# Performance work log

Measured on AMD Instinct MI355X. Metric: run time of the kernel, lower is better.

Reference implementation:

```python
import jax, jax.numpy as jnp
import numpy as np

B, C_IN, IMG, P = 64, 3, 224, 16
GRID = IMG // P              # 14
N_PATCH = GRID * GRID        # 196
S = N_PATCH + 1              # 197 tokens incl CLS
D, H, HD = 768, 12, 64
DFF = 3072
L, PRUNE_AFTER = 12, 4
RATIO, EPS = 0.5, 1e-6
NEG = -1e30                  # additive mask value (softmax weight -> exactly 0 in fp32)
N_CLASSES = 1000
N_KEEP = max(1, int(S * (1.0 - RATIO)))  # 98, matches torch topk count


def _ln(x, g, b):
    m = x.mean(-1, keepdims=True)
    v = ((x - m) ** 2).mean(-1, keepdims=True)
    return (x - m) * jax.lax.rsqrt(v + EPS) * g + b


def _attn(x, qkv_w, qkv_b, proj_w, proj_b, amask):
    Bx, N, C = x.shape
    qkv = (x @ qkv_w.T + qkv_b).reshape(Bx, N, 3, H, HD).transpose(2, 0, 3, 1, 4)
    q, k, v = qkv[0], qkv[1], qkv[2]            # [B,H,N,HD]
    s = jnp.einsum('bhqd,bhkd->bhqk', q, k) * (HD ** -0.5)
    if amask is not None:
        s = s + amask                            # [B,1,1,N] broadcast
    a = jax.nn.softmax(s, axis=-1)
    o = jnp.einsum('bhqk,bhkd->bhqd', a, v).transpose(0, 2, 1, 3).reshape(Bx, N, C)
    return o @ proj_w.T + proj_b


def _block(x, i, p, amask=None):
    h = _ln(x, p['ln1_g'][i], p['ln1_b'][i])
    x = x + _attn(h, p['qkv_w'][i], p['qkv_b'][i], p['proj_w'][i], p['proj_b'][i], amask)
    h = _ln(x, p['ln2_g'][i], p['ln2_b'][i])
    h = jax.nn.gelu(h @ p['fc1_w'][i].T + p['fc1_b'][i], approximate=False)
    x = x + (h @ p['fc2_w'][i].T + p['fc2_b'][i])
    return x


def _forward(images, patch_w, patch_b, cls_token, pos_embed,
             ln1_g, ln1_b, qkv_w, qkv_b, proj_w, proj_b,
             ln2_g, ln2_b, fc1_w, fc1_b, fc2_w, fc2_b,
             norm_g, norm_b, head_w, head_b):
    p = dict(ln1_g=ln1_g, ln1_b=ln1_b, qkv_w=qkv_w, qkv_b=qkv_b,
             proj_w=proj_w, proj_b=proj_b, ln2_g=ln2_g, ln2_b=ln2_b,
             fc1_w=fc1_w, fc1_b=fc1_b, fc2_w=fc2_w, fc2_b=fc2_b)
    Bx = images.shape[0]
    # patch embed: non-overlapping 16x16 conv == patch extract + matmul
    patches = images.reshape(Bx, C_IN, GRID, P, GRID, P).transpose(0, 2, 4, 1, 3, 5)
    patches = patches.reshape(Bx, N_PATCH, C_IN * P * P)
    x = patches @ patch_w.reshape(D, -1).T + patch_b          # [B,196,768]
    x = jnp.concatenate([jnp.broadcast_to(cls_token, (Bx, 1, D)), x], axis=1)
    x = x + pos_embed                                          # [B,197,768]
    # early dense blocks
    for i in range(PRUNE_AFTER):
        x = _block(x, i, p)
    # _threshold_prune: topk on token norms, CLS always kept
    scores = jnp.linalg.norm(x, axis=-1)                       # [B,S]
    _, idx = jax.lax.top_k(scores, N_KEEP)                     # [B,98]
    mask = jnp.zeros((Bx, S), bool).at[jnp.arange(Bx)[:, None], idx].set(True)
    mask = mask.at[:, 0].set(True)
    # _gather_pad: kept tokens compacted to front (original order), zeros after
    order = jnp.argsort(~mask, axis=1, stable=True)            # True positions first
    x_pad = jnp.take_along_axis(x, order[:, :, None], axis=1)
    attn_m = jnp.take_along_axis(mask, order, axis=1)          # [B,S] True-prefix
    x_pad = x_pad * attn_m[:, :, None]
    amask = jnp.where(attn_m, 0.0, NEG).astype(x.dtype)[:, None, None, :]  # [B,1,1,S]
    # late masked blocks
    for i in range(PRUNE_AFTER, L):
        x_pad = _block(x_pad, i, p, amask)
    cls = _ln(x_pad[:, 0], norm_g, norm_b)
    return cls @ head_w.T + head_b                             # [B,1000]


def setup_inputs():
    key = jax.random.key(0)
    ks = iter(jax.random.split(key, 32))
    r = lambda shape: jax.random.normal(next(ks), shape, jnp.float32) * 0.02
    return {
        'images': jax.random.normal(next(ks), (B, C_IN, IMG, IMG), jnp.float32),
        'patch_w': r((D, C_IN, P, P)),
        'patch_b': r((D,)),
        'cls_token': r((1, 1, D)),
        'pos_embed': r((1, S, D)),
        'ln1_g': jnp.ones((L, D), jnp.float32),
        'ln1_b': jnp.zeros((L, D), jnp.float32),
        'qkv_w': r((L, 3 * D, D)),
        'qkv_b': r((L, 3 * D)),
        'proj_w': r((L, D, D)),
        'proj_b': r((L, D)),
        'ln2_g': jnp.ones((L, D), jnp.float32),
        'ln2_b': jnp.zeros((L, D), jnp.float32),
        'fc1_w': r((L, DFF, D)),
        'fc1_b': r((L, DFF)),
        'fc2_w': r((L, D, DFF)),
        'fc2_b': r((L, D)),
        'norm_g': jnp.ones((D,), jnp.float32),
        'norm_b': jnp.zeros((D,), jnp.float32),
        'head_w': r((N_CLASSES, D)),
        'head_b': r((N_CLASSES,)),
    }


def reference(images, patch_w, patch_b, cls_token, pos_embed,
              ln1_g, ln1_b, qkv_w, qkv_b, proj_w, proj_b,
              ln2_g, ln2_b, fc1_w, fc1_b, fc2_w, fc2_b,
              norm_g, norm_b, head_w, head_b):
    return _forward(images, patch_w, patch_b, cls_token, pos_embed,
                    ln1_g, ln1_b, qkv_w, qkv_b, proj_w, proj_b,
                    ln2_g, ln2_b, fc1_w, fc1_b, fc2_w, fc2_b,
                    norm_g, norm_b, head_w, head_b)
```

## Files before the change

### kernel.cpp

```cpp
#include <hip/hip_runtime.h>
#include <cstdint>
#include <cstddef>


#define NTOK 197
#define NB 64
#define NHEAD 12
#define SL 99

typedef __attribute__((ext_vector_type(8))) _Float16 half8;
typedef __attribute__((ext_vector_type(4))) float f32x4;
typedef __attribute__((ext_vector_type(4))) unsigned short us4;

#define DEV static __device__ __forceinline__

DEV unsigned short f2h(float f) {
    union { _Float16 h; unsigned short u; } v;
    v.h = (_Float16)f;
    return v.u;
}
DEV float h2f(unsigned short u) {
    union { _Float16 h; unsigned short u; } v;
    v.u = u;
    return (float)v.h;
}

DEV void gload16(const void* g, void* l) {
    __builtin_amdgcn_global_load_lds((const __attribute__((address_space(1))) unsigned int*)g,
                                     (__attribute__((address_space(3))) unsigned int*)l, 16, 0, 0);
}

__global__ __launch_bounds__(256) void cvt_layer_k(const float* __restrict__ qw,
                                                   const float* __restrict__ pw,
                                                   const float* __restrict__ f1,
                                                   const float* __restrict__ f2,
                                                   unsigned short* __restrict__ dh)
{
    size_t t = (size_t)blockIdx.x * 256 + threadIdx.x;
    size_t e = t * 4;
    const float* src; size_t loc;
    if (e < 1769472)      { src = qw; loc = e; }
    else if (e < 2359296) { src = pw; loc = e - 1769472; }
    else if (e < 4718592) { src = f1; loc = e - 2359296; }
    else                  { src = f2; loc = e - 4718592; }
    float4 v = *(const float4*)(src + loc);
    us4 hi; hi.x = f2h(v.x); hi.y = f2h(v.y); hi.z = f2h(v.z); hi.w = f2h(v.w);
    *(us4*)(dh + e) = hi;
}

__global__ __launch_bounds__(256) void cvt_simple_k(const float* __restrict__ src,
                                                    unsigned short* __restrict__ dh, int n4)
{
    int t = blockIdx.x * 256 + threadIdx.x;
    if (t >= n4) return;
    size_t e = (size_t)t * 4;
    float4 v = *(const float4*)(src + e);
    us4 hi; hi.x = f2h(v.x); hi.y = f2h(v.y); hi.z = f2h(v.z); hi.w = f2h(v.w);
    *(us4*)(dh + e) = hi;
}

__global__ __launch_bounds__(256) void patch_extract2_k(const float* __restrict__ img,
                                                        unsigned short* __restrict__ ph)
{
    int pi = blockIdx.x, b = blockIdx.y;
    int gy = pi / 14, gx = pi % 14;
    size_t obase = ((size_t)b * 196 + pi) * 768;
    for (int f = threadIdx.x; f < 768; f += 256) {
        int c = f >> 8, py = (f >> 4) & 15, px = f & 15;
        float v = img[(((size_t)b * 3 + c) * 224 + gy * 16 + py) * 224 + gx * 16 + px];
        ph[obase + f] = f2h(v);
    }
}

__global__ __launch_bounds__(256) void assemble_k(const unsigned short* __restrict__ emb,
                                                  const float* __restrict__ cls,
                                                  const float* __restrict__ pos,
                                                  unsigned short* __restrict__ x)
{
    int s = blockIdx.x, b = blockIdx.y;
    size_t xo = ((size_t)b * NTOK + s) * 768;
    for (int d = threadIdx.x; d < 768; d += 256) {
        float v = (s == 0) ? cls[d] : h2f(emb[((size_t)b * 196 + (s - 1)) * 768 + d]);
        x[xo + d] = f2h(v + pos[(size_t)s * 768 + d]);
    }
}

__global__ __launch_bounds__(256) void ln2_k(const unsigned short* __restrict__ in,
                                             unsigned short* __restrict__ outh,
                                             const float* __restrict__ g,
                                             const float* __restrict__ bt, size_t ldin)
{
    const unsigned short* xr = in + (size_t)blockIdx.x * ldin;
    size_t ob = (size_t)blockIdx.x * 768;
    int t = threadIdx.x;
    float v0 = h2f(xr[t]), v1 = h2f(xr[t + 256]), v2 = h2f(xr[t + 512]);
    float s = v0 + v1 + v2;
#pragma unroll
    for (int o = 32; o; o >>= 1) s += __shfl_xor(s, o);
    __shared__ float r1[4], r2[4];
    int wv = t >> 6, ln = t & 63;
    if (ln == 0) r1[wv] = s;
    __syncthreads();
    float mean = (r1[0] + r1[1] + r1[2] + r1[3]) * (1.f / 768.f);
    float d0 = v0 - mean, d1 = v1 - mean, d2 = v2 - mean;
    float ss = d0 * d0 + d1 * d1 + d2 * d2;
#pragma unroll
    for (int o = 32; o; o >>= 1) ss += __shfl_xor(ss, o);
    if (ln == 0) r2[wv] = ss;
    __syncthreads();
    float inv = rsqrtf((r2[0] + r2[1] + r2[2] + r2[3]) * (1.f / 768.f) + 1e-6f);
    outh[ob + t]       = f2h(d0 * inv * g[t]       + bt[t]);
    outh[ob + t + 256] = f2h(d1 * inv * g[t + 256] + bt[t + 256]);
    outh[ob + t + 512] = f2h(d2 * inv * g[t + 512] + bt[t + 512]);
}

template<int EPI, int OS, int MAP>
__global__ __launch_bounds__(256) void mgemm_k(const unsigned short* __restrict__ Ah,
                                               const unsigned short* __restrict__ Wh,
                                               const float* __restrict__ bias,
                                               const unsigned short* __restrict__ res,
                                               unsigned short* __restrict__ Chi,
                                               float* __restrict__ Cf,
                                               int M, int N, int K, int nR, int nC, int nRmax)
{
    __shared__ unsigned short lds[3 * 8192];

    int rt, ct;
    {
        int bid = blockIdx.x;
        if (MAP == 0) { rt = bid % nR; ct = bid / nR; }
        else {
            int x = bid & 7, u = bid >> 3, rl, c;
            if (MAP == 2) { c = u % nC; rl = u / nC; }
            else          { rl = u % nRmax; c = u / nRmax; }
            rt = x + 8 * rl; ct = c;
            if (rt >= nR) return;
        }
    }
    const int row0 = rt << 7, col0 = ct << 7;
    const int tid = threadIdx.x;
    const int w = tid >> 6, lane = tid & 63;
    const int wr = w >> 1, wc = w & 1;
    const int srow = lane >> 2;
    const int schunk = ((lane & 3) ^ ((srow >> 1) & 3)) << 3;
    const int fr = lane & 15, fq = lane >> 4;
    const int rchunk = (fq ^ ((fr >> 1) & 3)) << 3;

    f32x4 acc[4][4];
#pragma unroll
    for (int m = 0; m < 4; m++)
#pragma unroll
        for (int n = 0; n < 4; n++) acc[m][n] = (f32x4)0.f;

    const int nk = K >> 5;

    auto stage = [&](int t, int slot) {
        const int k0 = t << 5;
        unsigned short* Ad = lds + slot * 8192;
        unsigned short* Bd = Ad + 4096;
#pragma unroll
        for (int i = 0; i < 2; i++) {
            int r = i * 64 + w * 16 + srow;
            int ga = row0 + r; if (ga > M - 1) ga = M - 1;
            int gb = col0 + r; if (gb > N - 1) gb = N - 1;
            gload16(Ah + (size_t)ga * K + k0 + schunk, Ad + i * 2048 + w * 512);
            gload16(Wh + (size_t)gb * K + k0 + schunk, Bd + i * 2048 + w * 512);
        }
    };

    stage(0, 0);
    stage(1, 1);
    int slot = 0, slot2 = 2;
    for (int t = 0; t < nk; ++t) {
        if (t + 1 < nk) asm volatile("s_waitcnt vmcnt(4)" ::: "memory");
        else            asm volatile("s_waitcnt vmcnt(0)" ::: "memory");
        __builtin_amdgcn_s_barrier();
        if (t + 2 < nk) stage(t + 2, slot2);
        const unsigned short* Ab = lds + slot * 8192;
        const unsigned short* Bb = Ab + 4096;
        half8 a[4], bb[4];
#pragma unroll
        for (int m = 0; m < 4; m++)
            a[m] = *(const half8*)(Ab + (wr * 64 + m * 16 + fr) * 32 + rchunk);
#pragma unroll
        for (int n = 0; n < 4; n++)
            bb[n] = *(const half8*)(Bb + (wc * 64 + n * 16 + fr) * 32 + rchunk);
#pragma unroll
        for (int m = 0; m < 4; m++)
#pragma unroll
            for (int n = 0; n < 4; n++)
                acc[m][n] = __builtin_amdgcn_mfma_f32_16x16x32_f16(a[m], bb[n], acc[m][n], 0, 0, 0);
        slot = (slot == 2) ? 0 : slot + 1;
        slot2 = (slot2 == 2) ? 0 : slot2 + 1;
    }

#pragma unroll
    for (int m = 0; m < 4; m++) {
#pragma unroll
        for (int n = 0; n < 4; n++) {
            int col = col0 + wc * 64 + n * 16 + fr;
#pragma unroll
            for (int r = 0; r < 4; r++) {
                int row = row0 + wr * 64 + m * 16 + fq * 4 + r;
                if (row < M && col < N) {
                    float v = acc[m][n][r] + bias[col];
                    size_t o = (size_t)row * N + col;
                    if (EPI == 2) v += h2f(res[o]);
                    if (EPI == 1) v = 0.5f * v * (1.f + erff(v * 0.70710678118654752f));
                    if (OS == 0) Cf[o] = v;
                    else Chi[o] = f2h(v);
                }
            }
        }
    }
}

template<int S, int KT, int PVKT, int PSTR>
__global__ __launch_bounds__(256) void attn2_k(const unsigned short* __restrict__ qh,
                                               unsigned short* __restrict__ oh,
                                               const int* __restrict__ cntp)
{
    constexpr int PVK = PVKT * 32;
    constexpr int QT = (S + 15) / 16;
    extern __shared__ unsigned short sh[];
    unsigned short* VT = sh;
    unsigned short* PL = sh + 64 * PSTR;

    const int h = blockIdx.x, b = blockIdx.y;
    const int tid = threadIdx.x, w = tid >> 6, lane = tid & 63;
    const int nk = cntp ? cntp[b] : S;
    const size_t qbase = (size_t)b * S * 2304 + (size_t)h * 64;
    const int fr = lane & 15, fq = lane >> 4;

    for (int j0 = 0; j0 < S; j0 += 32) {
        int j = j0 + (tid >> 3);
        int d8 = (tid & 7) * 8;
        if (j < S) {
            size_t src = qbase + (size_t)j * 2304 + 1536 + d8;
            us4 v0 = *(const us4*)(qh + src);
            us4 v1 = *(const us4*)(qh + src + 4);
            VT[(d8 + 0) * PSTR + j] = v0.x; VT[(d8 + 1) * PSTR + j] = v0.y;
            VT[(d8 + 2) * PSTR + j] = v0.z; VT[(d8 + 3) * PSTR + j] = v0.w;
            VT[(d8 + 4) * PSTR + j] = v1.x; VT[(d8 + 5) * PSTR + j] = v1.y;
            VT[(d8 + 6) * PSTR + j] = v1.z; VT[(d8 + 7) * PSTR + j] = v1.w;
        }
    }
    for (int idx = tid; idx < 64 * (PVK - S); idx += 256) {
        int d = idx / (PVK - S), j = S + idx % (PVK - S);
        VT[d * PSTR + j] = 0;
    }
    {
        unsigned short* Pw = PL + w * 16 * PSTR;
        for (int idx = lane; idx < 16 * (PVK - 16 * KT); idx += 64) {
            int rr = idx / (PVK - 16 * KT), cc = 16 * KT + idx % (PVK - 16 * KT);
            Pw[rr * PSTR + cc] = 0;
        }
    }
    __syncthreads();

    for (int qt = w; qt < QT; qt += 4) {
        int qr = qt * 16 + fr; int qrc = qr < S ? qr : S - 1;
        const size_t qrow = qbase + (size_t)qrc * 2304;
        half8 qf0[2];
#pragma unroll
        for (int ks = 0; ks < 2; ks++)
            qf0[ks] = *(const half8*)(qh + qrow + ks * 32 + fq * 8);
        f32x4 sc[KT];
#pragma unroll
        for (int kt = 0; kt < KT; kt++) {
            int ky = kt * 16 + fr; int kyc = ky < S ? ky : S - 1;
            const size_t krow = qbase + (size_t)kyc * 2304 + 768;
            f32x4 acc = (f32x4)0.f;
#pragma unroll
            for (int ks = 0; ks < 2; ks++) {
                half8 kh = *(const half8*)(qh + krow + ks * 32 + fq * 8);
                acc = __builtin_amdgcn_mfma_f32_16x16x32_f16(qf0[ks], kh, acc, 0, 0, 0);
            }
            sc[kt] = acc;
        }
        float mx[4] = {-3e38f, -3e38f, -3e38f, -3e38f};
#pragma unroll
        for (int kt = 0; kt < KT; kt++) {
            bool valid = (kt * 16 + fr) < nk;
#pragma unroll
            for (int r = 0; r < 4; r++) {
                float s = sc[kt][r] * 0.125f;
                sc[kt][r] = s;
                if (valid) mx[r] = fmaxf(mx[r], s);
            }
        }
#pragma unroll
        for (int off = 1; off < 16; off <<= 1)
#pragma unroll
            for (int r = 0; r < 4; r++) mx[r] = fmaxf(mx[r], __shfl_xor(mx[r], off));
        float sum[4] = {0.f, 0.f, 0.f, 0.f};
#pragma unroll
        for (int kt = 0; kt < KT; kt++) {
            bool valid = (kt * 16 + fr) < nk;
#pragma unroll
            for (int r = 0; r < 4; r++) {
                float p = valid ? __expf(sc[kt][r] - mx[r]) : 0.f;
                sc[kt][r] = p;
                sum[r] += p;
            }
        }
#pragma unroll
        for (int off = 1; off < 16; off <<= 1)
#pragma unroll
            for (int r = 0; r < 4; r++) sum[r] += __shfl_xor(sum[r], off);
        float inv[4];
#pragma unroll
        for (int r = 0; r < 4; r++) inv[r] = 1.f / sum[r];
        unsigned short* Pw = PL + w * 16 * PSTR;
#pragma unroll
        for (int kt = 0; kt < KT; kt++) {
#pragma unroll
            for (int r = 0; r < 4; r++)
                Pw[(fq * 4 + r) * PSTR + kt * 16 + fr] = f2h(sc[kt][r] * inv[r]);
        }
        f32x4 o[4];
#pragma unroll
        for (int n = 0; n < 4; n++) o[n] = (f32x4)0.f;
#pragma unroll
        for (int ks = 0; ks < PVKT; ks++) {
            half8 pa = *(const half8*)(Pw + fr * PSTR + ks * 32 + fq * 8);
#pragma unroll
            for (int n = 0; n < 4; n++) {
                half8 vb = *(const half8*)(VT + (n * 16 + fr) * PSTR + ks * 32 + fq * 8);
                o[n] = __builtin_amdgcn_mfma_f32_16x16x32_f16(pa, vb, o[n], 0, 0, 0);
            }
        }
#pragma unroll
        for (int n = 0; n < 4; n++) {
#pragma unroll
            for (int r = 0; r < 4; r++) {
                int row = qt * 16 + fq * 4 + r;
                if (row < S) {
                    size_t oidx = ((size_t)b * S + row) * 768 + (size_t)h * 64 + n * 16 + fr;
                    oh[oidx] = f2h(o[n][r]);
                }
            }
        }
    }
}

__global__ __launch_bounds__(256) void normsq_k(const unsigned short* __restrict__ x,
                                                float* __restrict__ norms)
{
    const unsigned short* xr = x + (size_t)blockIdx.x * 768;
    int t = threadIdx.x;
    float v0 = h2f(xr[t]), v1 = h2f(xr[t + 256]), v2 = h2f(xr[t + 512]);
    float ss = v0 * v0 + v1 * v1 + v2 * v2;
#pragma unroll
    for (int o = 32; o; o >>= 1) ss += __shfl_xor(ss, o);
    __shared__ float r1[4];
    if ((t & 63) == 0) r1[t >> 6] = ss;
    __syncthreads();
    if (t == 0) norms[blockIdx.x] = r1[0] + r1[1] + r1[2] + r1[3];
}

__global__ __launch_bounds__(256) void topk_k(const float* __restrict__ norms,
                                              int* __restrict__ idxmap, int* __restrict__ cnt)
{
    int b = blockIdx.x, t = threadIdx.x;
    __shared__ float n[NTOK];
    __shared__ unsigned char kp[NTOK];
    if (t < NTOK) n[t] = norms[b * NTOK + t];
    __syncthreads();
    if (t < NTOK) {
        float me = n[t];
        int rank = 0;
        for (int j = 0; j < NTOK; j++) rank += (n[j] > me) || (n[j] == me && j < t);
        kp[t] = (rank < 98) || (t == 0);
    }
    __syncthreads();
    if (t == 0) {
        int c = 0;
        for (int s = 0; s < NTOK; s++) if (kp[s]) idxmap[b * SL + c++] = s;
        cnt[b] = c;
        for (int j = c; j < SL; j++) idxmap[b * SL + j] = 0;
    }
}

__global__ __launch_bounds__(256) void gather_k(const unsigned short* __restrict__ x,
                                                const int* __restrict__ idxmap,
                                                const int* __restrict__ cnt,
                                                unsigned short* __restrict__ xl)
{
    int j = blockIdx.x, b = blockIdx.y;
    size_t dst = ((size_t)b * SL + j) * 768;
    if (j < cnt[b]) {
        int s = idxmap[b * SL + j];
        size_t src = ((size_t)b * NTOK + s) * 768;
        for (int d = threadIdx.x; d < 768; d += 256) xl[dst + d] = x[src + d];
    } else {
        for (int d = threadIdx.x; d < 768; d += 256) xl[dst + d] = 0;
    }
}

extern "C" void kernel_launch(void* const* d_in, const int* in_sizes, int n_in,
                              void* d_out, int out_size, void* d_ws, size_t ws_size,
                              hipStream_t stream)
{
    const float* images  = (const float*)d_in[0];
    const float* patch_w = (const float*)d_in[1];
    const float* patch_b = (const float*)d_in[2];
    const float* cls_tok = (const float*)d_in[3];
    const float* pos_emb = (const float*)d_in[4];
    const float* ln1_g   = (const float*)d_in[5];
    const float* ln1_b   = (const float*)d_in[6];
    const float* qkv_w   = (const float*)d_in[7];
    const float* qkv_b   = (const float*)d_in[8];
    const float* proj_w  = (const float*)d_in[9];
    const float* proj_b  = (const float*)d_in[10];
    const float* ln2_g   = (const float*)d_in[11];
    const float* ln2_b   = (const float*)d_in[12];
    const float* fc1_w   = (const float*)d_in[13];
    const float* fc1_b   = (const float*)d_in[14];
    const float* fc2_w   = (const float*)d_in[15];
    const float* fc2_b   = (const float*)d_in[16];
    const float* norm_g  = (const float*)d_in[17];
    const float* norm_b  = (const float*)d_in[18];
    const float* head_w  = (const float*)d_in[19];
    const float* head_b  = (const float*)d_in[20];
    float* outp = (float*)d_out;

    char* W = (char*)d_ws;
    unsigned short* x16  = (unsigned short*)W;
    unsigned short* hbh  = (unsigned short*)(W + 19365888);
    char* R = W + 38731776;
    unsigned short* ph   = (unsigned short*)R;
    unsigned short* emb  = (unsigned short*)(R + 19365888);
    unsigned short* qkh  = (unsigned short*)R;
    unsigned short* ffh  = (unsigned short*)R;
    unsigned short* xl16 = (unsigned short*)(W + 116195328);
    unsigned short* wbh  = (unsigned short*)(W + 125927424);
    unsigned short* pwh  = (unsigned short*)(W + 140083200);
    unsigned short* hwb  = (unsigned short*)(W + 141262848);
    float* norms         = (float*)(W + 142835712);
    unsigned short* clsb = (unsigned short*)(W + 142886912);
    int* idxmap          = (int*)(W + 142985216);
    int* cnt             = (int*)(W + 143010560);

    const int LDS_EARLY = (64 * 232 + 4 * 16 * 232) * 2;
    const int LDS_LATE  = (64 * 136 + 4 * 16 * 136) * 2;
    (void)hipFuncSetAttribute(reinterpret_cast<const void*>(&attn2_k<197, 13, 7, 232>),
                              hipFuncAttributeMaxDynamicSharedMemorySize, LDS_EARLY);
    (void)hipFuncSetAttribute(reinterpret_cast<const void*>(&attn2_k<99, 7, 4, 136>),
                              hipFuncAttributeMaxDynamicSharedMemorySize, LDS_LATE);

    const int nR1 = 99, nRm1 = 13;
    const int nRp = 98, nRmp = 13;
    const int nR2 = 50, nRm2 = 7;

    cvt_simple_k<<<576, 256, 0, stream>>>(patch_w, pwh, 147456);
    patch_extract2_k<<<dim3(196, NB), 256, 0, stream>>>(images, ph);
    mgemm_k<0, 1, 2><<<8 * nRmp * 6, 256, 0, stream>>>(ph, pwh, patch_b, nullptr,
        emb, nullptr, 12544, 768, 768, nRp, 6, nRmp);
    assemble_k<<<dim3(NTOK, NB), 256, 0, stream>>>(emb, cls_tok, pos_emb, x16);

    const int M1 = NB * NTOK;
    for (int i = 0; i < 4; i++) {
        cvt_layer_k<<<6912, 256, 0, stream>>>(qkv_w + (size_t)i * 1769472, proj_w + (size_t)i * 589824,
                                              fc1_w + (size_t)i * 2359296, fc2_w + (size_t)i * 2359296,
                                              wbh);
        ln2_k<<<M1, 256, 0, stream>>>(x16, hbh, ln1_g + (size_t)i * 768, ln1_b + (size_t)i * 768, 768);
        mgemm_k<0, 1, 1><<<8 * nRm1 * 18, 256, 0, stream>>>(hbh, wbh,
            qkv_b + (size_t)i * 2304, nullptr, qkh, nullptr, M1, 2304, 768, nR1, 18, nRm1);
        attn2_k<197, 13, 7, 232><<<dim3(NHEAD, NB), 256, LDS_EARLY, stream>>>(qkh, hbh, nullptr);
        mgemm_k<2, 1, 2><<<8 * nRm1 * 6, 256, 0, stream>>>(hbh, wbh + 1769472,
            proj_b + (size_t)i * 768, x16, x16, nullptr, M1, 768, 768, nR1, 6, nRm1);
        ln2_k<<<M1, 256, 0, stream>>>(x16, hbh, ln2_g + (size_t)i * 768, ln2_b + (size_t)i * 768, 768);
        mgemm_k<1, 1, 1><<<8 * nRm1 * 24, 256, 0, stream>>>(hbh, wbh + 2359296,
            fc1_b + (size_t)i * 3072, nullptr, ffh, nullptr, M1, 3072, 768, nR1, 24, nRm1);
        mgemm_k<2, 1, 2><<<8 * nRm1 * 6, 256, 0, stream>>>(ffh, wbh + 4718592,
            fc2_b + (size_t)i * 768, x16, x16, nullptr, M1, 768, 3072, nR1, 6, nRm1);
    }

    normsq_k<<<M1, 256, 0, stream>>>(x16, norms);
    topk_k<<<NB, 256, 0, stream>>>(norms, idxmap, cnt);
    gather_k<<<dim3(SL, NB), 256, 0, stream>>>(x16, idxmap, cnt, xl16);

    const int M2 = NB * SL;
    for (int i = 4; i < 12; i++) {
        cvt_layer_k<<<6912, 256, 0, stream>>>(qkv_w + (size_t)i * 1769472, proj_w + (size_t)i * 589824,
                                              fc1_w + (size_t)i * 2359296, fc2_w + (size_t)i * 2359296,
                                              wbh);
        ln2_k<<<M2, 256, 0, stream>>>(xl16, hbh, ln1_g + (size_t)i * 768, ln1_b + (size_t)i * 768, 768);
        mgemm_k<0, 1, 1><<<8 * nRm2 * 18, 256, 0, stream>>>(hbh, wbh,
            qkv_b + (size_t)i * 2304, nullptr, qkh, nullptr, M2, 2304, 768, nR2, 18, nRm2);
        attn2_k<99, 7, 4, 136><<<dim3(NHEAD, NB), 256, LDS_LATE, stream>>>(qkh, hbh, cnt);
        mgemm_k<2, 1, 2><<<8 * nRm2 * 6, 256, 0, stream>>>(hbh, wbh + 1769472,
            proj_b + (size_t)i * 768, xl16, xl16, nullptr, M2, 768, 768, nR2, 6, nRm2);
        ln2_k<<<M2, 256, 0, stream>>>(xl16, hbh, ln2_g + (size_t)i * 768, ln2_b + (size_t)i * 768, 768);
        mgemm_k<1, 1, 1><<<8 * nRm2 * 24, 256, 0, stream>>>(hbh, wbh + 2359296,
            fc1_b + (size_t)i * 3072, nullptr, ffh, nullptr, M2, 3072, 768, nR2, 24, nRm2);
        mgemm_k<2, 1, 2><<<8 * nRm2 * 6, 256, 0, stream>>>(ffh, wbh + 4718592,
            fc2_b + (size_t)i * 768, xl16, xl16, nullptr, M2, 768, 3072, nR2, 6, nRm2);
    }

    ln2_k<<<NB, 256, 0, stream>>>(xl16, clsb, norm_g, norm_b, (size_t)SL * 768);
    cvt_simple_k<<<750, 256, 0, stream>>>(head_w, hwb, 192000);
    mgemm_k<0, 0, 0><<<8, 256, 0, stream>>>(clsb, hwb,
        head_b, nullptr, nullptr, outp, 64, 1000, 768, 1, 8, 1);
}
```

Baseline: 3.866 ms.

## Batch weight conversion four layers at a time and remap GEMM tiles to contiguous XCD row blocks

Weight fp32->fp16 conversion now runs once per group of four layers into a larger workspace buffer instead of once per layer, cutting kernel launches and letting the GEMMs read from separate per-layer buffers. The GEMM block-to-tile mapping changes so each XCD (blockIdx & 7) owns a contiguous range of row tiles rather than an interleaved stride-8 set. This is meant to improve L2 locality of A-rows on each chiplet. It costs more workspace memory and fewer, larger conversion launches.

```diff
diff --git a/kernel.cpp b/kernel.cpp
--- a/kernel.cpp
+++ b/kernel.cpp
@@ -30,22 +30,26 @@
                                      (__attribute__((address_space(3))) unsigned int*)l, 16, 0, 0);
 }
 
-__global__ __launch_bounds__(256) void cvt_layer_k(const float* __restrict__ qw,
-                                                   const float* __restrict__ pw,
-                                                   const float* __restrict__ f1,
-                                                   const float* __restrict__ f2,
-                                                   unsigned short* __restrict__ dh)
-{
-    size_t t = (size_t)blockIdx.x * 256 + threadIdx.x;
+__global__ __launch_bounds__(256) void cvt_layer4_k(const float* __restrict__ qw,
+                                                    const float* __restrict__ pw,
+                                                    const float* __restrict__ f1,
+                                                    const float* __restrict__ f2,
+                                                    int i0,
+                                                    unsigned short* __restrict__ dst)
+{
+    int l = blockIdx.x / 6912;
+    int b2 = blockIdx.x % 6912;
+    int li = i0 + l;
+    size_t t = (size_t)b2 * 256 + threadIdx.x;
     size_t e = t * 4;
     const float* src; size_t loc;
-    if (e < 1769472)      { src = qw; loc = e; }
-    else if (e < 2359296) { src = pw; loc = e - 1769472; }
-    else if (e < 4718592) { src = f1; loc = e - 2359296; }
-    else                  { src = f2; loc = e - 4718592; }
+    if (e < 1769472)      { src = qw + (size_t)li * 1769472; loc = e; }
+    else if (e < 2359296) { src = pw + (size_t)li * 589824;  loc = e - 1769472; }
+    else if (e < 4718592) { src = f1 + (size_t)li * 2359296; loc = e - 2359296; }
+    else                  { src = f2 + (size_t)li * 2359296; loc = e - 4718592; }
     float4 v = *(const float4*)(src + loc);
     us4 hi; hi.x = f2h(v.x); hi.y = f2h(v.y); hi.z = f2h(v.z); hi.w = f2h(v.w);
-    *(us4*)(dh + e) = hi;
+    *(us4*)(dst + (size_t)l * 7077888 + e) = hi;
 }
 
 __global__ __launch_bounds__(256) void cvt_simple_k(const float* __restrict__ src,
@@ -121,7 +125,7 @@
                                                const unsigned short* __restrict__ res,
                                                unsigned short* __restrict__ Chi,
                                                float* __restrict__ Cf,
-                                               int M, int N, int K, int nR, int nC, int nRmax)
+                                               int M, int N, int K, int nR, int nC, int nRloc)
 {
     __shared__ unsigned short lds[3 * 8192];
 
@@ -130,10 +134,10 @@
         int bid = blockIdx.x;
         if (MAP == 0) { rt = bid % nR; ct = bid / nR; }
         else {
-            int x = bid & 7, u = bid >> 3, rl, c;
-            if (MAP == 2) { c = u % nC; rl = u / nC; }
-            else          { rl = u % nRmax; c = u / nRmax; }
-            rt = x + 8 * rl; ct = c;
+            int xcd = bid & 7, u = bid >> 3, rl, c;
+            if (MAP == 3) { rl = u % nRloc; c = u / nRloc; }
+            else          { c = u % nC;     rl = u / nC;   }
+            rt = xcd * nRloc + rl; ct = c;
             if (rt >= nR) return;
         }
     }
@@ -434,13 +438,13 @@
     unsigned short* qkh  = (unsigned short*)R;
     unsigned short* ffh  = (unsigned short*)R;
     unsigned short* xl16 = (unsigned short*)(W + 116195328);
-    unsigned short* wbh  = (unsigned short*)(W + 125927424);
-    unsigned short* pwh  = (unsigned short*)(W + 140083200);
-    unsigned short* hwb  = (unsigned short*)(W + 141262848);
-    float* norms         = (float*)(W + 142835712);
-    unsigned short* clsb = (unsigned short*)(W + 142886912);
-    int* idxmap          = (int*)(W + 142985216);
-    int* cnt             = (int*)(W + 143010560);
+    unsigned short* wb4  = (unsigned short*)(W + 125927424);
+    unsigned short* pwh  = (unsigned short*)(W + 182550528);
+    unsigned short* hwb  = (unsigned short*)(W + 183730176);
+    float* norms         = (float*)(W + 185303040);
+    unsigned short* clsb = (unsigned short*)(W + 185353472);
+    int* idxmap          = (int*)(W + 185451776);
+    int* cnt             = (int*)(W + 185477120);
 
     const int LDS_EARLY = (64 * 232 + 4 * 16 * 232) * 2;
     const int LDS_LATE  = (64 * 136 + 4 * 16 * 136) * 2;
@@ -449,32 +453,32 @@
     (void)hipFuncSetAttribute(reinterpret_cast<const void*>(&attn2_k<99, 7, 4, 136>),
                               hipFuncAttributeMaxDynamicSharedMemorySize, LDS_LATE);
 
-    const int nR1 = 99, nRm1 = 13;
-    const int nRp = 98, nRmp = 13;
-    const int nR2 = 50, nRm2 = 7;
+    const int nR1 = 99, nRl1 = 13;
+    const int nRp = 98, nRlp = 13;
+    const int nR2 = 50, nRl2 = 7;
 
     cvt_simple_k<<<576, 256, 0, stream>>>(patch_w, pwh, 147456);
     patch_extract2_k<<<dim3(196, NB), 256, 0, stream>>>(images, ph);
-    mgemm_k<0, 1, 2><<<8 * nRmp * 6, 256, 0, stream>>>(ph, pwh, patch_b, nullptr,
-        emb, nullptr, 12544, 768, 768, nRp, 6, nRmp);
+    mgemm_k<0, 1, 3><<<8 * nRlp * 6, 256, 0, stream>>>(ph, pwh, patch_b, nullptr,
+        emb, nullptr, 12544, 768, 768, nRp, 6, nRlp);
     assemble_k<<<dim3(NTOK, NB), 256, 0, stream>>>(emb, cls_tok, pos_emb, x16);
 
     const int M1 = NB * NTOK;
     for (int i = 0; i < 4; i++) {
-        cvt_layer_k<<<6912, 256, 0, stream>>>(qkv_w + (size_t)i * 1769472, proj_w + (size_t)i * 589824,
-                                              fc1_w + (size_t)i * 2359296, fc2_w + (size_t)i * 2359296,
-                                              wbh);
+        if (i == 0)
+            cvt_layer4_k<<<4 * 6912, 256, 0, stream>>>(qkv_w, proj_w, fc1_w, fc2_w, 0, wb4);
+        unsigned short* wbh = wb4 + (size_t)(i & 3) * 7077888;
         ln2_k<<<M1, 256, 0, stream>>>(x16, hbh, ln1_g + (size_t)i * 768, ln1_b + (size_t)i * 768, 768);
-        mgemm_k<0, 1, 1><<<8 * nRm1 * 18, 256, 0, stream>>>(hbh, wbh,
-            qkv_b + (size_t)i * 2304, nullptr, qkh, nullptr, M1, 2304, 768, nR1, 18, nRm1);
+        mgemm_k<0, 1, 3><<<8 * nRl1 * 18, 256, 0, stream>>>(hbh, wbh,
+            qkv_b + (size_t)i * 2304, nullptr, qkh, nullptr, M1, 2304, 768, nR1, 18, nRl1);
         attn2_k<197, 13, 7, 232><<<dim3(NHEAD, NB), 256, LDS_EARLY, stream>>>(qkh, hbh, nullptr);
-        mgemm_k<2, 1, 2><<<8 * nRm1 * 6, 256, 0, stream>>>(hbh, wbh + 1769472,
-            proj_b + (size_t)i * 768, x16, x16, nullptr, M1, 768, 768, nR1, 6, nRm1);
+        mgemm_k<2, 1, 3><<<8 * nRl1 * 6, 256, 0, stream>>>(hbh, wbh + 1769472,
+            proj_b + (size_t)i * 768, x16, x16, nullptr, M1, 768, 768, nR1, 6, nRl1);
         ln2_k<<<M1, 256, 0, stream>>>(x16, hbh, ln2_g + (size_t)i * 768, ln2_b + (size_t)i * 768, 768);
-        mgemm_k<1, 1, 1><<<8 * nRm1 * 24, 256, 0, stream>>>(hbh, wbh + 2359296,
-            fc1_b + (size_t)i * 3072, nullptr, ffh, nullptr, M1, 3072, 768, nR1, 24, nRm1);
-        mgemm_k<2, 1, 2><<<8 * nRm1 * 6, 256, 0, stream>>>(ffh, wbh + 4718592,
-            fc2_b + (size_t)i * 768, x16, x16, nullptr, M1, 768, 3072, nR1, 6, nRm1);
+        mgemm_k<1, 1, 3><<<8 * nRl1 * 24, 256, 0, stream>>>(hbh, wbh + 2359296,
+            fc1_b + (size_t)i * 3072, nullptr, ffh, nullptr, M1, 3072, 768, nR1, 24, nRl1);
+        mgemm_k<2, 1, 4><<<8 * nRl1 * 6, 256, 0, stream>>>(ffh, wbh + 4718592,
+            fc2_b + (size_t)i * 768, x16, x16, nullptr, M1, 768, 3072, nR1, 6, nRl1);
     }
 
     normsq_k<<<M1, 256, 0, stream>>>(x16, norms);
@@ -483,20 +487,22 @@
 
     const int M2 = NB * SL;
     for (int i = 4; i < 12; i++) {
-        cvt_layer_k<<<6912, 256, 0, stream>>>(qkv_w + (size_t)i * 1769472, proj_w + (size_t)i * 589824,
-                                              fc1_w + (size_t)i * 2359296, fc2_w + (size_t)i * 2359296,
-                                              wbh);
+        if (i == 4)
+            cvt_layer4_k<<<4 * 6912, 256, 0, stream>>>(qkv_w, proj_w, fc1_w, fc2_w, 4, wb4);
+        if (i == 8)
+            cvt_layer4_k<<<4 * 6912, 256, 0, stream>>>(qkv_w, proj_w, fc1_w, fc2_w, 8, wb4);
+        unsigned short* wbh = wb4 + (size_t)(i & 3) * 7077888;
         ln2_k<<<M2, 256, 0, stream>>>(xl16, hbh, ln1_g + (size_t)i * 768, ln1_b + (size_t)i * 768, 768);
-        mgemm_k<0, 1, 1><<<8 * nRm2 * 18, 256, 0, stream>>>(hbh, wbh,
-            qkv_b + (size_t)i * 2304, nullptr, qkh, nullptr, M2, 2304, 768, nR2, 18, nRm2);
+        mgemm_k<0, 1, 3><<<8 * nRl2 * 18, 256, 0, stream>>>(hbh, wbh,
+            qkv_b + (size_t)i * 2304, nullptr, qkh, nullptr, M2, 2304, 768, nR2, 18, nRl2);
         attn2_k<99, 7, 4, 136><<<dim3(NHEAD, NB), 256, LDS_LATE, stream>>>(qkh, hbh, cnt);
-        mgemm_k<2, 1, 2><<<8 * nRm2 * 6, 256, 0, stream>>>(hbh, wbh + 1769472,
-            proj_b + (size_t)i * 768, xl16, xl16, nullptr, M2, 768, 768, nR2, 6, nRm2);
+        mgemm_k<2, 1, 3><<<8 * nRl2 * 6, 256, 0, stream>>>(hbh, wbh + 1769472,
+            proj_b + (size_t)i * 768, xl16, xl16, nullptr, M2, 768, 768, nR2, 6, nRl2);
         ln2_k<<<M2, 256, 0, stream>>>(xl16, hbh, ln2_g + (size_t)i * 768, ln2_b + (size_t)i * 768, 768);
-        mgemm_k<1, 1, 1><<<8 * nRm2 * 24, 256, 0, stream>>>(hbh, wbh + 2359296,
-            fc1_b + (size_t)i * 3072, nullptr, ffh, nullptr, M2, 3072, 768, nR2, 24, nRm2);
-        mgemm_k<2, 1, 2><<<8 * nRm2 * 6, 256, 0, stream>>>(ffh, wbh + 4718592,
-            fc2_b + (size_t)i * 768, xl16, xl16, nullptr, M2, 768, 3072, nR2, 6, nRm2);
+        mgemm_k<1, 1, 3><<<8 * nRl2 * 24, 256, 0, stream>>>(hbh, wbh + 2359296,
+            fc1_b + (size_t)i * 3072, nullptr, ffh, nullptr, M2, 3072, 768, nR2, 24, nRl2);
+        mgemm_k<2, 1, 4><<<8 * nRl2 * 6, 256, 0, stream>>>(ffh, wbh + 4718592,
+            fc2_b + (size_t)i * 768, xl16, xl16, nullptr, M2, 768, 3072, nR2, 6, nRl2);
     }
 
     ln2_k<<<NB, 256, 0, stream>>>(xl16, clsb, norm_g, norm_b, (size_t)SL * 768);
```

Result: no change. 3.846 ms (-0.5%).
